# Kernel tuning notes

Hardware: AMD Instinct MI355X
Metric: run time of the kernel (lower is better)

## Reference

```python
import jax, jax.numpy as jnp
import numpy as np

RGB2GRAY = jnp.array([0.299, 0.587, 0.114], dtype=jnp.float32)


def _trilinear_slice(grid, z, y, x):
    """grid: (F, L, GH, GW); z,y,x: (H, W) float positions in index space
    (align_corners=True convention). Returns (H, W, F)."""
    F_, L, GH, GW = grid.shape
    z = jnp.clip(z, 0.0, L - 1)
    y = jnp.clip(y, 0.0, GH - 1)
    x = jnp.clip(x, 0.0, GW - 1)
    z0 = jnp.floor(z).astype(jnp.int32); z1 = jnp.minimum(z0 + 1, L - 1)
    y0 = jnp.floor(y).astype(jnp.int32); y1 = jnp.minimum(y0 + 1, GH - 1)
    x0 = jnp.floor(x).astype(jnp.int32); x1 = jnp.minimum(x0 + 1, GW - 1)
    wz = (z - z0)[..., None]  # (H, W, 1)
    wy = (y - y0)[..., None]
    wx = (x - x0)[..., None]

    def g(zi, yi, xi):  # gather corner -> (H, W, F)
        return jnp.moveaxis(grid[:, zi, yi, xi], 0, -1)

    c00 = g(z0, y0, x0) * (1 - wx) + g(z0, y0, x1) * wx
    c01 = g(z0, y1, x0) * (1 - wx) + g(z0, y1, x1) * wx
    c10 = g(z1, y0, x0) * (1 - wx) + g(z1, y0, x1) * wx
    c11 = g(z1, y1, x0) * (1 - wx) + g(z1, y1, x1) * wx
    c0 = c00 * (1 - wy) + c01 * wy
    c1 = c10 * (1 - wy) + c11 * wy
    return c0 * (1 - wz) + c1 * wz


def setup_inputs() -> dict:
    key = jax.random.key(0)
    k = jax.random.split(key, 5)
    H, W = 1080, 1920
    N, F_, L, GH, GW = 50, 16, 8, 16, 16
    hidden = 64
    rgb = jax.random.uniform(k[0], (H, W, 3), dtype=jnp.float32)
    grids = jax.random.normal(k[1], (N, F_, L, GH, GW), dtype=jnp.float32) * 0.1
    W1 = jax.random.normal(k[2], (hidden, F_), dtype=jnp.float32) * (1.0 / np.sqrt(F_))
    W2 = jax.random.normal(k[3], (hidden, hidden), dtype=jnp.float32) * (1.0 / np.sqrt(hidden))
    W3 = jax.random.normal(k[4], (12, hidden), dtype=jnp.float32) * (1.0 / np.sqrt(hidden))
    return {"rgb": rgb, "grids": grids, "W1": W1, "W2": W2, "W3": W3, "cam_idx": 3}


def reference(rgb, grids, W1, W2, W3, cam_idx):
    H, W, _ = rgb.shape
    _, F_, L, GH, GW = grids.shape
    grid = grids[cam_idx]  # (F, L, GH, GW)
    # guidance: gray in [0,1]; grid_sample coords in [-1,1] with align_corners=True
    # map directly to index space: pos = coord01 * (size - 1)
    gray = jnp.clip(jnp.tensordot(rgb, RGB2GRAY, axes=([-1], [0])), 0.0, 1.0)  # (H, W)
    gy = jnp.linspace(0.0, 1.0, H, dtype=jnp.float32)[:, None]  # (H, 1)
    gx = jnp.linspace(0.0, 1.0, W, dtype=jnp.float32)[None, :]  # (1, W)
    z = gray * (L - 1)
    y = jnp.broadcast_to(gy * (GH - 1), (H, W))
    x = jnp.broadcast_to(gx * (GW - 1), (H, W))
    feat = _trilinear_slice(grid, z, y, x)  # (H, W, F)
    # tiny per-pixel MLP (bias-free, torch Linear applies x @ W.T)
    h = jnp.tanh(feat @ W1.T)
    h = jnp.tanh(h @ W2.T)
    out = h @ W3.T  # (H, W, 12)
    return out.reshape(1, H, W, 3, 4)
```

## Files before the change

kernel.cpp:

```cpp
#include <hip/hip_runtime.h>

#define H_IMG 1080
#define W_IMG 1920
#define NPIX (H_IMG * W_IMG)

typedef __attribute__((ext_vector_type(8))) short bfrag8;
typedef __attribute__((ext_vector_type(4))) float facc4;

#define PK2_OFF 131072
#define PK3_OFF 147456
#define PK1_OFF 151552

__device__ __forceinline__ void split_bf16(float x, unsigned short& hi, unsigned short& lo) {
    unsigned xu = __float_as_uint(x);
    hi = (unsigned short)(xu >> 16);
    float hif = __uint_as_float(xu & 0xffff0000u);
    float lof = x - hif;
    lo = (unsigned short)(__float_as_uint(lof) >> 16);
}

__global__ void prep_kernel(const float* __restrict__ grids,
                            const int* __restrict__ cam_idx,
                            const float* __restrict__ W1,
                            const float* __restrict__ W2,
                            const float* __restrict__ W3,
                            float* __restrict__ grid_t,
                            unsigned short* __restrict__ pk1,
                            unsigned short* __restrict__ pk2,
                            unsigned short* __restrict__ pk3) {
    int idx = blockIdx.x * 256 + threadIdx.x;
    {
        int f = idx & 15, x = (idx >> 4) & 15, y = (idx >> 8) & 15, z = (idx >> 12) & 7;
        int cam = cam_idx[0];
        grid_t[idx] = grids[(((cam * 16 + f) * 8 + z) * 16 + y) * 16 + x];
    }
    if (idx < 8192) {
        int i = idx & 7, lane = (idx >> 3) & 63, h = (idx >> 9) & 1,
            s = (idx >> 10) & 1, nt = (idx >> 11) & 3;
        int j = nt * 16 + (lane & 15);
        int k = s * 32 + (lane >> 4) * 8 + i;
        unsigned short hi, lo;
        split_bf16(W2[j * 64 + k], hi, lo);
        pk2[idx] = h ? lo : hi;
    } else if (idx < 10240) {
        int e = idx - 8192;
        int i = e & 7, lane = (e >> 3) & 63, h = (e >> 9) & 1, s = (e >> 10) & 1;
        int c = lane & 15;
        int k = s * 32 + (lane >> 4) * 8 + i;
        float x = (c < 12) ? W3[c * 64 + k] : 0.0f;
        unsigned short hi, lo;
        split_bf16(x, hi, lo);
        pk3[e] = h ? lo : hi;
    } else if (idx < 14336) {
        int e = idx - 10240;
        int i = e & 7, lane = (e >> 3) & 63, h = (e >> 9) & 1, nt = (e >> 10) & 3;
        int j = nt * 16 + (lane & 15);
        int k = (lane >> 4) * 8 + i;
        float x = (k < 16) ? W1[j * 16 + k] : 0.0f;
        unsigned short hi, lo;
        split_bf16(x, hi, lo);
        pk1[e] = h ? lo : hi;
    }
}

__device__ __forceinline__ float fast_tanh(float x) {
    float e = __expf(2.0f * x);
    return 1.0f - 2.0f * __builtin_amdgcn_rcpf(e + 1.0f);
}

__device__ __forceinline__ unsigned pack2(float x) {
    unsigned xu = __float_as_uint(x);
    float lof = x - __uint_as_float(xu & 0xffff0000u);
    return __builtin_amdgcn_perm(__float_as_uint(lof), xu, 0x07060302u);
}

__device__ __forceinline__ bfrag8 frag_hi(uint4 q0, uint4 q1) {
    uint4 r;
    r.x = __builtin_amdgcn_perm(q0.y, q0.x, 0x05040100u);
    r.y = __builtin_amdgcn_perm(q0.w, q0.z, 0x05040100u);
    r.z = __builtin_amdgcn_perm(q1.y, q1.x, 0x05040100u);
    r.w = __builtin_amdgcn_perm(q1.w, q1.z, 0x05040100u);
    return __builtin_bit_cast(bfrag8, r);
}
__device__ __forceinline__ bfrag8 frag_lo(uint4 q0, uint4 q1) {
    uint4 r;
    r.x = __builtin_amdgcn_perm(q0.y, q0.x, 0x07060302u);
    r.y = __builtin_amdgcn_perm(q0.w, q0.z, 0x07060302u);
    r.z = __builtin_amdgcn_perm(q1.y, q1.x, 0x07060302u);
    r.w = __builtin_amdgcn_perm(q1.w, q1.z, 0x07060302u);
    return __builtin_bit_cast(bfrag8, r);
}

#define DS_FENCE() asm volatile("s_waitcnt lgkmcnt(0)" ::: "memory")

__global__ __launch_bounds__(256, 3)
void nbat_main(const float* __restrict__ rgb,
               const float* __restrict__ grid_t,
               const unsigned short* __restrict__ pk1,
               const unsigned short* __restrict__ pk2,
               const unsigned short* __restrict__ pk3,
               float* __restrict__ out) {
    __shared__ __align__(16) unsigned hbuf[4][2048];

    const int tid = threadIdx.x;
    const int w = tid >> 6, l = tid & 63;
    const int g = l >> 4, cc = l & 15;
    unsigned* hb = hbuf[w];
    uint4* hb4 = (uint4*)hb;

    const int pixbase = blockIdx.x * 256 + w * 64;
    const int pix = pixbase + l;
    const int row = pix / W_IMG;
    const int col = pix - row * W_IMG;

    const bfrag8* pk1v = (const bfrag8*)pk1;
    bfrag8 b1h[4], b1l[4];
#pragma unroll
    for (int nt = 0; nt < 4; ++nt) {
        b1h[nt] = pk1v[(nt * 2 + 0) * 64 + l];
        b1l[nt] = pk1v[(nt * 2 + 1) * 64 + l];
    }

    float r = rgb[3 * pix + 0];
    float gch = rgb[3 * pix + 1];
    float b = rgb[3 * pix + 2];
    float gray = fminf(fmaxf(0.299f * r + 0.587f * gch + 0.114f * b, 0.0f), 1.0f);

    float z = fminf(fmaxf(gray * 7.0f, 0.0f), 7.0f);
    float y = (float)row * (15.0f / 1079.0f);
    float x = (float)col * (15.0f / 1919.0f);

    float zf = floorf(z), yf = floorf(y), xf = floorf(x);
    int z0 = (int)zf, y0 = (int)yf, x0 = (int)xf;
    int z1 = min(z0 + 1, 7), y1 = min(y0 + 1, 15), x1 = min(x0 + 1, 15);
    float wz = z - zf, wy = y - yf, wx = x - xf;

    float feat[16];
#pragma unroll
    for (int i = 0; i < 16; ++i) feat[i] = 0.0f;

    const float4* gt4 = (const float4*)grid_t;
#pragma unroll
    for (int cz = 0; cz < 2; ++cz) {
        int zz = cz ? z1 : z0;
        float wwz = cz ? wz : (1.0f - wz);
#pragma unroll
        for (int cy = 0; cy < 2; ++cy) {
            int yy = cy ? y1 : y0;
            float wwzy = wwz * (cy ? wy : (1.0f - wy));
#pragma unroll
            for (int cx = 0; cx < 2; ++cx) {
                int xx = cx ? x1 : x0;
                float wc = wwzy * (cx ? wx : (1.0f - wx));
                int base = ((zz * 16 + yy) * 16 + xx) * 4;
#pragma unroll
                for (int q = 0; q < 4; ++q) {
                    float4 v = gt4[base + q];
                    feat[4 * q + 0] = fmaf(wc, v.x, feat[4 * q + 0]);
                    feat[4 * q + 1] = fmaf(wc, v.y, feat[4 * q + 1]);
                    feat[4 * q + 2] = fmaf(wc, v.z, feat[4 * q + 2]);
                    feat[4 * q + 3] = fmaf(wc, v.w, feat[4 * q + 3]);
                }
            }
        }
    }

#pragma unroll
    for (int ch = 0; ch < 4; ++ch) {
        uint4 q;
        q.x = pack2(feat[4 * ch + 0]);
        q.y = pack2(feat[4 * ch + 1]);
        q.z = pack2(feat[4 * ch + 2]);
        q.w = pack2(feat[4 * ch + 3]);
        hb4[l * 4 + (ch ^ (l & 3))] = q;
    }
    DS_FENCE();

    facc4 acc1[4][4];
#pragma unroll
    for (int mt = 0; mt < 4; ++mt)
#pragma unroll
        for (int nt = 0; nt < 4; ++nt) acc1[mt][nt] = (facc4){0.f, 0.f, 0.f, 0.f};

#pragma unroll
    for (int mt = 0; mt < 4; ++mt) {
        int rr_ = mt * 16 + cc;
        uint4 q0 = hb4[rr_ * 4 + ((2 * (g & 1) + 0) ^ (rr_ & 3))];
        uint4 q1 = hb4[rr_ * 4 + ((2 * (g & 1) + 1) ^ (rr_ & 3))];
        bfrag8 ah = frag_hi(q0, q1);
        bfrag8 al = frag_lo(q0, q1);
#pragma unroll
        for (int nt = 0; nt < 4; ++nt) {
            acc1[mt][nt] = __builtin_amdgcn_mfma_f32_16x16x32_bf16(al, b1h[nt], acc1[mt][nt], 0, 0, 0);
            acc1[mt][nt] = __builtin_amdgcn_mfma_f32_16x16x32_bf16(ah, b1l[nt], acc1[mt][nt], 0, 0, 0);
            acc1[mt][nt] = __builtin_amdgcn_mfma_f32_16x16x32_bf16(ah, b1h[nt], acc1[mt][nt], 0, 0, 0);
        }
    }
    DS_FENCE();

    const bfrag8* pk2v = (const bfrag8*)pk2;
    facc4 acc2[4][4];
#pragma unroll
    for (int mt = 0; mt < 4; ++mt)
#pragma unroll
        for (int nt = 0; nt < 4; ++nt) acc2[mt][nt] = (facc4){0.f, 0.f, 0.f, 0.f};

#pragma unroll
    for (int s = 0; s < 2; ++s) {
        bfrag8 b2h[4], b2l[4];
#pragma unroll
        for (int nt = 0; nt < 4; ++nt) {
            b2h[nt] = pk2v[((nt * 2 + s) * 2 + 0) * 64 + l];
            b2l[nt] = pk2v[((nt * 2 + s) * 2 + 1) * 64 + l];
        }
#pragma unroll
        for (int ntl = 0; ntl < 2; ++ntl) {
            int nt = 2 * s + ntl;
#pragma unroll
            for (int mt = 0; mt < 4; ++mt)
#pragma unroll
                for (int rr = 0; rr < 4; ++rr) {
                    float t = fast_tanh(acc1[mt][nt][rr]);
                    int rrow = mt * 16 + g * 4 + rr;
                    int colv = ntl * 16 + cc;
                    hb[rrow * 32 + ((((colv >> 2) ^ (rrow & 7)) << 2) | (colv & 3))] = pack2(t);
                }
        }
        DS_FENCE();
#pragma unroll
        for (int mt = 0; mt < 4; ++mt) {
            int rr_ = mt * 16 + cc;
            uint4 q0 = hb4[rr_ * 8 + ((2 * g + 0) ^ (rr_ & 7))];
            uint4 q1 = hb4[rr_ * 8 + ((2 * g + 1) ^ (rr_ & 7))];
            bfrag8 ah = frag_hi(q0, q1);
            bfrag8 al = frag_lo(q0, q1);
#pragma unroll
            for (int nt = 0; nt < 4; ++nt) {
                acc2[mt][nt] = __builtin_amdgcn_mfma_f32_16x16x32_bf16(al, b2h[nt], acc2[mt][nt], 0, 0, 0);
                acc2[mt][nt] = __builtin_amdgcn_mfma_f32_16x16x32_bf16(ah, b2l[nt], acc2[mt][nt], 0, 0, 0);
                acc2[mt][nt] = __builtin_amdgcn_mfma_f32_16x16x32_bf16(ah, b2h[nt], acc2[mt][nt], 0, 0, 0);
            }
        }
        DS_FENCE();
    }

    const bfrag8* pk3v = (const bfrag8*)pk3;
    facc4 o3[4];
#pragma unroll
    for (int mt = 0; mt < 4; ++mt) o3[mt] = (facc4){0.f, 0.f, 0.f, 0.f};

#pragma unroll
    for (int s = 0; s < 2; ++s) {
        bfrag8 b3h = pk3v[(s * 2 + 0) * 64 + l];
        bfrag8 b3l = pk3v[(s * 2 + 1) * 64 + l];
#pragma unroll
        for (int ntl = 0; ntl < 2; ++ntl) {
            int nt = 2 * s + ntl;
#pragma unroll
            for (int mt = 0; mt < 4; ++mt)
#pragma unroll
                for (int rr = 0; rr < 4; ++rr) {
                    float t = fast_tanh(acc2[mt][nt][rr]);
                    int rrow = mt * 16 + g * 4 + rr;
                    int colv = ntl * 16 + cc;
                    hb[rrow * 32 + ((((colv >> 2) ^ (rrow & 7)) << 2) | (colv & 3))] = pack2(t);
                }
        }
        DS_FENCE();
#pragma unroll
        for (int mt = 0; mt < 4; ++mt) {
            int rr_ = mt * 16 + cc;
            uint4 q0 = hb4[rr_ * 8 + ((2 * g + 0) ^ (rr_ & 7))];
            uint4 q1 = hb4[rr_ * 8 + ((2 * g + 1) ^ (rr_ & 7))];
            bfrag8 ah = frag_hi(q0, q1);
            bfrag8 al = frag_lo(q0, q1);
            o3[mt] = __builtin_amdgcn_mfma_f32_16x16x32_bf16(al, b3h, o3[mt], 0, 0, 0);
            o3[mt] = __builtin_amdgcn_mfma_f32_16x16x32_bf16(ah, b3l, o3[mt], 0, 0, 0);
            o3[mt] = __builtin_amdgcn_mfma_f32_16x16x32_bf16(ah, b3h, o3[mt], 0, 0, 0);
        }
        DS_FENCE();
    }

    if (cc < 12) {
#pragma unroll
        for (int mt = 0; mt < 4; ++mt)
#pragma unroll
            for (int rr = 0; rr < 4; ++rr) {
                int p = pixbase + mt * 16 + g * 4 + rr;
                out[p * 12 + cc] = o3[mt][rr];
            }
    }
}

extern "C" void kernel_launch(void* const* d_in, const int* in_sizes, int n_in,
                              void* d_out, int out_size, void* d_ws, size_t ws_size,
                              hipStream_t stream) {
    const float* rgb   = (const float*)d_in[0];
    const float* grids = (const float*)d_in[1];
    const float* W1    = (const float*)d_in[2];
    const float* W2    = (const float*)d_in[3];
    const float* W3    = (const float*)d_in[4];
    const int*   cam   = (const int*)d_in[5];

    float* grid_t = (float*)d_ws;
    unsigned short* pk2 = (unsigned short*)((char*)d_ws + PK2_OFF);
    unsigned short* pk3 = (unsigned short*)((char*)d_ws + PK3_OFF);
    unsigned short* pk1 = (unsigned short*)((char*)d_ws + PK1_OFF);

    hipLaunchKernelGGL(prep_kernel, dim3(128), dim3(256), 0, stream,
                       grids, cam, W1, W2, W3, grid_t, pk1, pk2, pk3);
    hipLaunchKernelGGL(nbat_main, dim3(NPIX / 256), dim3(256), 0, stream,
                       rgb, grid_t, pk1, pk2, pk3, (float*)d_out);
}
```

Before: 163.8 us.

## Transpose MLP so weights are A operand and pixels are B operand

After: 150.5 us. 8.1% less time.

```diff
diff --git a/kernel.cpp b/kernel.cpp
--- a/kernel.cpp
+++ b/kernel.cpp
@@ -36,8 +36,8 @@
     }
     if (idx < 8192) {
         int i = idx & 7, lane = (idx >> 3) & 63, h = (idx >> 9) & 1,
-            s = (idx >> 10) & 1, nt = (idx >> 11) & 3;
-        int j = nt * 16 + (lane & 15);
+            s = (idx >> 10) & 1, mt = (idx >> 11) & 3;
+        int j = mt * 16 + (lane & 15);
         int k = s * 32 + (lane >> 4) * 8 + i;
         unsigned short hi, lo;
         split_bf16(W2[j * 64 + k], hi, lo);
@@ -53,8 +53,8 @@
         pk3[e] = h ? lo : hi;
     } else if (idx < 14336) {
         int e = idx - 10240;
-        int i = e & 7, lane = (e >> 3) & 63, h = (e >> 9) & 1, nt = (e >> 10) & 3;
-        int j = nt * 16 + (lane & 15);
+        int i = e & 7, lane = (e >> 3) & 63, h = (e >> 9) & 1, mt = (e >> 10) & 3;
+        int j = mt * 16 + (lane & 15);
         int k = (lane >> 4) * 8 + i;
         float x = (k < 16) ? W1[j * 16 + k] : 0.0f;
         unsigned short hi, lo;
@@ -68,30 +68,12 @@
     return 1.0f - 2.0f * __builtin_amdgcn_rcpf(e + 1.0f);
 }
 
-__device__ __forceinline__ unsigned pack2(float x) {
-    unsigned xu = __float_as_uint(x);
-    float lof = x - __uint_as_float(xu & 0xffff0000u);
-    return __builtin_amdgcn_perm(__float_as_uint(lof), xu, 0x07060302u);
-}
-
-__device__ __forceinline__ bfrag8 frag_hi(uint4 q0, uint4 q1) {
-    uint4 r;
-    r.x = __builtin_amdgcn_perm(q0.y, q0.x, 0x05040100u);
-    r.y = __builtin_amdgcn_perm(q0.w, q0.z, 0x05040100u);
-    r.z = __builtin_amdgcn_perm(q1.y, q1.x, 0x05040100u);
-    r.w = __builtin_amdgcn_perm(q1.w, q1.z, 0x05040100u);
-    return __builtin_bit_cast(bfrag8, r);
-}
-__device__ __forceinline__ bfrag8 frag_lo(uint4 q0, uint4 q1) {
-    uint4 r;
-    r.x = __builtin_amdgcn_perm(q0.y, q0.x, 0x07060302u);
-    r.y = __builtin_amdgcn_perm(q0.w, q0.z, 0x07060302u);
-    r.z = __builtin_amdgcn_perm(q1.y, q1.x, 0x07060302u);
-    r.w = __builtin_amdgcn_perm(q1.w, q1.z, 0x07060302u);
-    return __builtin_bit_cast(bfrag8, r);
+__device__ __forceinline__ unsigned pack_hi_pair(float e, float o) {
+    return __builtin_amdgcn_perm(__float_as_uint(o), __float_as_uint(e), 0x07060302u);
 }
 
 #define DS_FENCE() asm volatile("s_waitcnt lgkmcnt(0)" ::: "memory")
+#define MFMA16(A, B, C) __builtin_amdgcn_mfma_f32_16x16x32_bf16((A), (B), (C), 0, 0, 0)
 
 __global__ __launch_bounds__(256, 3)
 void nbat_main(const float* __restrict__ rgb,
@@ -113,14 +95,6 @@
     const int row = pix / W_IMG;
     const int col = pix - row * W_IMG;
 
-    const bfrag8* pk1v = (const bfrag8*)pk1;
-    bfrag8 b1h[4], b1l[4];
-#pragma unroll
-    for (int nt = 0; nt < 4; ++nt) {
-        b1h[nt] = pk1v[(nt * 2 + 0) * 64 + l];
-        b1l[nt] = pk1v[(nt * 2 + 1) * 64 + l];
-    }
-
     float r = rgb[3 * pix + 0];
     float gch = rgb[3 * pix + 1];
     float b = rgb[3 * pix + 2];
@@ -165,35 +139,67 @@
         }
     }
 
-#pragma unroll
-    for (int ch = 0; ch < 4; ++ch) {
-        uint4 q;
-        q.x = pack2(feat[4 * ch + 0]);
-        q.y = pack2(feat[4 * ch + 1]);
-        q.z = pack2(feat[4 * ch + 2]);
-        q.w = pack2(feat[4 * ch + 3]);
-        hb4[l * 4 + (ch ^ (l & 3))] = q;
+    const int sl = (l >> 1) & 3;
+    {
+        uint4 q0, q1;
+        q0.x = pack_hi_pair(feat[0], feat[1]);
+        q0.y = pack_hi_pair(feat[2], feat[3]);
+        q0.z = pack_hi_pair(feat[4], feat[5]);
+        q0.w = pack_hi_pair(feat[6], feat[7]);
+        q1.x = pack_hi_pair(feat[8], feat[9]);
+        q1.y = pack_hi_pair(feat[10], feat[11]);
+        q1.z = pack_hi_pair(feat[12], feat[13]);
+        q1.w = pack_hi_pair(feat[14], feat[15]);
+        uint4 zz4 = make_uint4(0u, 0u, 0u, 0u);
+        hb4[l * 4 + (0 ^ sl)] = q0;
+        hb4[l * 4 + (1 ^ sl)] = q1;
+        hb4[l * 4 + (2 ^ sl)] = zz4;
+        hb4[l * 4 + (3 ^ sl)] = zz4;
     }
     DS_FENCE();
 
+    auto transition = [&](const facc4& v, int mtl, int nt) __attribute__((always_inline)) {
+        float t0 = fast_tanh(v[0]);
+        float t1 = fast_tanh(v[1]);
+        float t2 = fast_tanh(v[2]);
+        float t3 = fast_tanh(v[3]);
+        unsigned hA = pack_hi_pair(t0, t1);
+        unsigned hB = pack_hi_pair(t2, t3);
+        float l0 = t0 - __uint_as_float(hA << 16);
+        float l1 = t1 - __uint_as_float(hA & 0xffff0000u);
+        float l2 = t2 - __uint_as_float(hB << 16);
+        float l3 = t3 - __uint_as_float(hB & 0xffff0000u);
+        unsigned lA = pack_hi_pair(l0, l1);
+        unsigned lB = pack_hi_pair(l2, l3);
+        int p = cc + 16 * nt;
+        int u = p * 16 + ((((mtl << 1) + (g >> 1)) ^ ((p >> 1) & 3)) << 2) + ((g & 1) << 1);
+        *(uint2*)(hb + u) = make_uint2(hA, hB);
+        *(uint2*)(hb + 1024 + u) = make_uint2(lA, lB);
+    };
+
+    const bfrag8* pk1v = (const bfrag8*)pk1;
     facc4 acc1[4][4];
 #pragma unroll
     for (int mt = 0; mt < 4; ++mt)
 #pragma unroll
         for (int nt = 0; nt < 4; ++nt) acc1[mt][nt] = (facc4){0.f, 0.f, 0.f, 0.f};
-
-#pragma unroll
-    for (int mt = 0; mt < 4; ++mt) {
-        int rr_ = mt * 16 + cc;
-        uint4 q0 = hb4[rr_ * 4 + ((2 * (g & 1) + 0) ^ (rr_ & 3))];
-        uint4 q1 = hb4[rr_ * 4 + ((2 * (g & 1) + 1) ^ (rr_ & 3))];
-        bfrag8 ah = frag_hi(q0, q1);
-        bfrag8 al = frag_lo(q0, q1);
+    {
+        bfrag8 w1h[4], w1l[4];
+#pragma unroll
+        for (int mt = 0; mt < 4; ++mt) {
+            w1h[mt] = pk1v[(mt * 2 + 0) * 64 + l];
+            w1l[mt] = pk1v[(mt * 2 + 1) * 64 + l];
+        }
 #pragma unroll
         for (int nt = 0; nt < 4; ++nt) {
-            acc1[mt][nt] = __builtin_amdgcn_mfma_f32_16x16x32_bf16(al, b1h[nt], acc1[mt][nt], 0, 0, 0);
-            acc1[mt][nt] = __builtin_amdgcn_mfma_f32_16x16x32_bf16(ah, b1l[nt], acc1[mt][nt], 0, 0, 0);
-            acc1[mt][nt] = __builtin_amdgcn_mfma_f32_16x16x32_bf16(ah, b1h[nt], acc1[mt][nt], 0, 0, 0);
+            int p = cc + 16 * nt;
+            uint4 bq = hb4[p * 4 + (g ^ ((p >> 1) & 3))];
+            bfrag8 bf = __builtin_bit_cast(bfrag8, bq);
+#pragma unroll
+            for (int mt = 0; mt < 4; ++mt) {
+                acc1[mt][nt] = MFMA16(w1l[mt], bf, acc1[mt][nt]);
+                acc1[mt][nt] = MFMA16(w1h[mt], bf, acc1[mt][nt]);
+            }
         }
     }
     DS_FENCE();
@@ -207,38 +213,30 @@
 
 #pragma unroll
     for (int s = 0; s < 2; ++s) {
-        bfrag8 b2h[4], b2l[4];
+#pragma unroll
+        for (int mtl = 0; mtl < 2; ++mtl)
+#pragma unroll
+            for (int nt = 0; nt < 4; ++nt) transition(acc1[2 * s + mtl][nt], mtl, nt);
+        DS_FENCE();
+        bfrag8 w2h[4], w2l[4];
+#pragma unroll
+        for (int mt = 0; mt < 4; ++mt) {
+            w2h[mt] = pk2v[((mt * 2 + s) * 2 + 0) * 64 + l];
+            w2l[mt] = pk2v[((mt * 2 + s) * 2 + 1) * 64 + l];
+        }
 #pragma unroll
         for (int nt = 0; nt < 4; ++nt) {
-            b2h[nt] = pk2v[((nt * 2 + s) * 2 + 0) * 64 + l];
-            b2l[nt] = pk2v[((nt * 2 + s) * 2 + 1) * 64 + l];
-        }
-#pragma unroll
-        for (int ntl = 0; ntl < 2; ++ntl) {
-            int nt = 2 * s + ntl;
-#pragma unroll
-            for (int mt = 0; mt < 4; ++mt)
-#pragma unroll
-                for (int rr = 0; rr < 4; ++rr) {
-                    float t = fast_tanh(acc1[mt][nt][rr]);
-                    int rrow = mt * 16 + g * 4 + rr;
-                    int colv = ntl * 16 + cc;
-                    hb[rrow * 32 + ((((colv >> 2) ^ (rrow & 7)) << 2) | (colv & 3))] = pack2(t);
-                }
-        }
-        DS_FENCE();
-#pragma unroll
-        for (int mt = 0; mt < 4; ++mt) {
-            int rr_ = mt * 16 + cc;
-            uint4 q0 = hb4[rr_ * 8 + ((2 * g + 0) ^ (rr_ & 7))];
-            uint4 q1 = hb4[rr_ * 8 + ((2 * g + 1) ^ (rr_ & 7))];
-            bfrag8 ah = frag_hi(q0, q1);
-            bfrag8 al = frag_lo(q0, q1);
-#pragma unroll
-            for (int nt = 0; nt < 4; ++nt) {
-                acc2[mt][nt] = __builtin_amdgcn_mfma_f32_16x16x32_bf16(al, b2h[nt], acc2[mt][nt], 0, 0, 0);
-                acc2[mt][nt] = __builtin_amdgcn_mfma_f32_16x16x32_bf16(ah, b2l[nt], acc2[mt][nt], 0, 0, 0);
-                acc2[mt][nt] = __builtin_amdgcn_mfma_f32_16x16x32_bf16(ah, b2h[nt], acc2[mt][nt], 0, 0, 0);
+            int p = cc + 16 * nt;
+            int sw = (p >> 1) & 3;
+            uint4 qh = hb4[p * 4 + (g ^ sw)];
+            uint4 ql = hb4[256 + p * 4 + (g ^ sw)];
+            bfrag8 bh = __builtin_bit_cast(bfrag8, qh);
+            bfrag8 bl = __builtin_bit_cast(bfrag8, ql);
+#pragma unroll
+            for (int mt = 0; mt < 4; ++mt) {
+                acc2[mt][nt] = MFMA16(w2h[mt], bl, acc2[mt][nt]);
+                acc2[mt][nt] = MFMA16(w2l[mt], bh, acc2[mt][nt]);
+                acc2[mt][nt] = MFMA16(w2h[mt], bh, acc2[mt][nt]);
             }
         }
         DS_FENCE();
@@ -247,48 +245,39 @@
     const bfrag8* pk3v = (const bfrag8*)pk3;
     facc4 o3[4];
 #pragma unroll
-    for (int mt = 0; mt < 4; ++mt) o3[mt] = (facc4){0.f, 0.f, 0.f, 0.f};
+    for (int nt = 0; nt < 4; ++nt) o3[nt] = (facc4){0.f, 0.f, 0.f, 0.f};
 
 #pragma unroll
     for (int s = 0; s < 2; ++s) {
-        bfrag8 b3h = pk3v[(s * 2 + 0) * 64 + l];
-        bfrag8 b3l = pk3v[(s * 2 + 1) * 64 + l];
-#pragma unroll
-        for (int ntl = 0; ntl < 2; ++ntl) {
-            int nt = 2 * s + ntl;
-#pragma unroll
-            for (int mt = 0; mt < 4; ++mt)
-#pragma unroll
-                for (int rr = 0; rr < 4; ++rr) {
-                    float t = fast_tanh(acc2[mt][nt][rr]);
-                    int rrow = mt * 16 + g * 4 + rr;
-                    int colv = ntl * 16 + cc;
-                    hb[rrow * 32 + ((((colv >> 2) ^ (rrow & 7)) << 2) | (colv & 3))] = pack2(t);
-                }
-        }
+#pragma unroll
+        for (int mtl = 0; mtl < 2; ++mtl)
+#pragma unroll
+            for (int nt = 0; nt < 4; ++nt) transition(acc2[2 * s + mtl][nt], mtl, nt);
         DS_FENCE();
-#pragma unroll
-        for (int mt = 0; mt < 4; ++mt) {
-            int rr_ = mt * 16 + cc;
-            uint4 q0 = hb4[rr_ * 8 + ((2 * g + 0) ^ (rr_ & 7))];
-            uint4 q1 = hb4[rr_ * 8 + ((2 * g + 1) ^ (rr_ & 7))];
-            bfrag8 ah = frag_hi(q0, q1);
-            bfrag8 al = frag_lo(q0, q1);
-            o3[mt] = __builtin_amdgcn_mfma_f32_16x16x32_bf16(al, b3h, o3[mt], 0, 0, 0);
-            o3[mt] = __builtin_amdgcn_mfma_f32_16x16x32_bf16(ah, b3l, o3[mt], 0, 0, 0);
-            o3[mt] = __builtin_amdgcn_mfma_f32_16x16x32_bf16(ah, b3h, o3[mt], 0, 0, 0);
-        }
-        DS_FENCE();
-    }
-
-    if (cc < 12) {
-#pragma unroll
-        for (int mt = 0; mt < 4; ++mt)
-#pragma unroll
-            for (int rr = 0; rr < 4; ++rr) {
-                int p = pixbase + mt * 16 + g * 4 + rr;
-                out[p * 12 + cc] = o3[mt][rr];
-            }
+        bfrag8 w3h = pk3v[(s * 2 + 0) * 64 + l];
+        bfrag8 w3l = pk3v[(s * 2 + 1) * 64 + l];
+#pragma unroll
+        for (int nt = 0; nt < 4; ++nt) {
+            int p = cc + 16 * nt;
+            int sw = (p >> 1) & 3;
+            uint4 qh = hb4[p * 4 + (g ^ sw)];
+            uint4 ql = hb4[256 + p * 4 + (g ^ sw)];
+            bfrag8 bh = __builtin_bit_cast(bfrag8, qh);
+            bfrag8 bl = __builtin_bit_cast(bfrag8, ql);
+            o3[nt] = MFMA16(w3h, bl, o3[nt]);
+            o3[nt] = MFMA16(w3l, bh, o3[nt]);
+            o3[nt] = MFMA16(w3h, bh, o3[nt]);
+        }
+        if (s == 0) DS_FENCE();
+    }
+
+    if (g < 3) {
+#pragma unroll
+        for (int nt = 0; nt < 4; ++nt) {
+            int p = pixbase + 16 * nt + cc;
+            *(float4*)(out + p * 12 + 4 * g) =
+                make_float4(o3[nt][0], o3[nt][1], o3[nt][2], o3[nt][3]);
+        }
     }
 }
 
```
